# Performance work log

Hardware: AMD Instinct MI355X
Metric: run time of the kernel (lower is better)

## Reference

```python
import jax, jax.numpy as jnp
import numpy as np

H, D, EF, NT, ET = 4, 32, 32, 4, 8
N, E = 100000, 1600000
NEG_SLOPE = 0.2


def setup_inputs() -> dict:
    key = jax.random.key(0)
    ks = jax.random.split(key, 11)
    return {
        "feat": jax.random.normal(ks[0], (N, H * D), jnp.float32),
        "fc": jax.random.normal(ks[1], (NT, H, D), jnp.float32) * 0.1,
        "edge_emb": jax.random.normal(ks[2], (ET, EF), jnp.float32),
        "W_e": jax.random.normal(ks[3], (H * EF, EF), jnp.float32) * 0.1,
        "attn_l": jax.random.normal(ks[4], (1, H, D), jnp.float32) * 0.1,
        "attn_r": jax.random.normal(ks[5], (1, H, D), jnp.float32) * 0.1,
        "attn_e": jax.random.normal(ks[6], (1, H, EF), jnp.float32) * 0.1,
        "node_types": jax.random.randint(ks[7], (N,), 0, NT, jnp.int32),
        "e_feat": jax.random.randint(ks[8], (E,), 0, ET, jnp.int32),
        "src": jax.random.randint(ks[9], (E,), 0, N, jnp.int32),
        "dst": jax.random.randint(ks[10], (E,), 0, N, jnp.int32),
    }


def reference(feat, fc, edge_emb, W_e, attn_l, attn_r, attn_e, node_types, e_feat, src, dst):
    n = feat.shape[0]
    h = feat.reshape(n, H, D)                      # [N,H,D] (h_src == h_dst)
    fs = h * fc[node_types]                        # per-node-type scaling, feat_src == feat_dst

    # edge-type embedding path: Embedding -> Linear(edge_feats, H*edge_feats) -> attn_e score
    emb = (edge_emb @ W_e.T).reshape(ET, H, EF)    # [ET,H,EF]
    ee = (emb * attn_e).sum(-1)[e_feat]            # [E,H]

    el = (fs * attn_l).sum(-1)                     # [N,H]
    er = (fs * attn_r).sum(-1)                     # [N,H]
    e = jax.nn.leaky_relu(el[src] + er[dst] + ee, NEG_SLOPE)  # [E,H]

    # edge_softmax: segment softmax over destination node
    m = jax.ops.segment_max(e, dst, num_segments=n)           # [N,H]
    ex = jnp.exp(e - m[dst])
    s = jax.ops.segment_sum(ex, dst, num_segments=n)          # [N,H]
    a = ex / s[dst]                                            # [E,H]

    # u_mul_e + sum aggregation
    msg = fs[src] * a[:, :, None]                              # [E,H,D]
    rst = jax.ops.segment_sum(msg, dst, num_segments=n)       # [N,H,D]

    rst = rst + h                                              # residual (Identity, in==out feats)
    return rst, a[:, :, None]
```

## Files before the change

kernel.cpp:

```cpp
#include <hip/hip_runtime.h>
#include <stdint.h>

namespace {
constexpr int kH = 4, kD = 32, kEF = 32, kNT = 4, kET = 8;
constexpr int kHD = kH * kD;
constexpr float kNegSlope = 0.2f;
constexpr int kNB = 782;
constexpr int kHB = 512;
constexpr int kXP = 20;

using f32x2 = __attribute__((ext_vector_type(2))) float;

__device__ __forceinline__ float lrelu(float x) { return x > 0.f ? x : kNegSlope * x; }

__global__ void __launch_bounds__(256) k_init(
    const float* __restrict__ feat, const float* __restrict__ fc,
    const float* __restrict__ edge_emb, const float* __restrict__ W_e,
    const float* __restrict__ attn_l, const float* __restrict__ attn_r,
    const float* __restrict__ attn_e, const int* __restrict__ node_types,
    float* __restrict__ el, float* __restrict__ er, uint8_t* __restrict__ fs,
    float* __restrict__ ee_tab, int N) {
  if (blockIdx.x == 0 && threadIdx.x < kET * kH) {
    int et = threadIdx.x / kH, h = threadIdx.x % kH;
    float acc = 0.f;
    for (int f = 0; f < kEF; ++f) {
      const float* wrow = W_e + (h * kEF + f) * kEF;
      const float* erow = edge_emb + et * kEF;
      float emb = 0.f;
      for (int k = 0; k < kEF; ++k) emb += erow[k] * wrow[k];
      acc += emb * attn_e[h * kEF + f];
    }
    ee_tab[et * kH + h] = acc;
  }
  int gid = blockIdx.x * blockDim.x + threadIdx.x;
  int node = gid >> 5;
  int lane = threadIdx.x & 31;
  if (node >= N) return;
  int nt = node_types[node];
  float4 f4 = *(const float4*)(feat + (size_t)(node << 7) + lane * 4);
  float4 c4 = *(const float4*)(fc + nt * kHD + lane * 4);
  float4 al = *(const float4*)(attn_l + lane * 4);
  float4 ar = *(const float4*)(attn_r + lane * 4);
  float fx = f4.x * c4.x, fy = f4.y * c4.y, fz = f4.z * c4.z, fw = f4.w * c4.w;
  int w = __builtin_amdgcn_cvt_pk_fp8_f32(fx, fy, 0, false);
  w = __builtin_amdgcn_cvt_pk_fp8_f32(fz, fw, w, true);
  *(int*)(fs + (size_t)(node << 7) + lane * 4) = w;
  float pl = fx * al.x + fy * al.y + fz * al.z + fw * al.w;
  float pr = fx * ar.x + fy * ar.y + fz * ar.z + fw * ar.w;
#pragma unroll
  for (int off = 1; off < 8; off <<= 1) {
    pl += __shfl_xor(pl, off);
    pr += __shfl_xor(pr, off);
  }
  if ((lane & 7) == 0) {
    int h = lane >> 3;
    el[node * kH + h] = pl;
    er[node * kH + h] = pr;
  }
}

__global__ void __launch_bounds__(256) k_hist(const int* __restrict__ dst,
                                              int* __restrict__ partial, int E) {
  __shared__ int h[kNB];
  for (int i = threadIdx.x; i < kNB; i += 256) h[i] = 0;
  __syncthreads();
  int per = (E + gridDim.x - 1) / gridDim.x;
  int e0 = blockIdx.x * per;
  int e1 = min(e0 + per, E);
  for (int i = e0 + threadIdx.x; i < e1; i += 256) atomicAdd(&h[dst[i] >> 7], 1);
  __syncthreads();
  for (int i = threadIdx.x; i < kNB; i += 256) partial[blockIdx.x * kNB + i] = h[i];
}

__global__ void __launch_bounds__(256) k_scanA(int* __restrict__ partial,
                                               int* __restrict__ btot) {
  __shared__ int bufa[kHB], bufb[kHB];
  int b = blockIdx.x, t = threadIdx.x;
  bufa[t] = partial[t * kNB + b];
  bufa[t + 256] = partial[(t + 256) * kNB + b];
  __syncthreads();
  int* cur = bufa;
  int* nxt = bufb;
  for (int off = 1; off < kHB; off <<= 1) {
    for (int i = t; i < kHB; i += 256) nxt[i] = cur[i] + (i >= off ? cur[i - off] : 0);
    __syncthreads();
    int* sw = cur; cur = nxt; nxt = sw;
  }
  partial[t * kNB + b] = t ? cur[t - 1] : 0;
  partial[(t + 256) * kNB + b] = cur[t + 255];
  if (t == 0) btot[b] = cur[kHB - 1];
}

__global__ void __launch_bounds__(1024) k_scanB(const int* __restrict__ btot,
                                                int* __restrict__ bbase) {
  __shared__ int bufa[1024], bufb[1024];
  int t = threadIdx.x;
  bufa[t] = (t < kNB) ? btot[t] : 0;
  __syncthreads();
  int* cur = bufa;
  int* nxt = bufb;
  for (int off = 1; off < 1024; off <<= 1) {
    nxt[t] = cur[t] + (t >= off ? cur[t - off] : 0);
    __syncthreads();
    int* sw = cur; cur = nxt; nxt = sw;
  }
  if (t < kNB) bbase[t] = t ? cur[t - 1] : 0;
  if (t == kNB - 1) bbase[kNB] = cur[t];
}

__global__ void __launch_bounds__(256) k_scatter2(
    const int* __restrict__ dst, const int* __restrict__ src,
    const int* __restrict__ e_feat, const int* __restrict__ partial,
    const int* __restrict__ bbase, int* __restrict__ tmp, int E) {
  __shared__ int h[kNB];
  for (int i = threadIdx.x; i < kNB; i += 256) h[i] = 0;
  __syncthreads();
  int per = (E + gridDim.x - 1) / gridDim.x;
  int e0 = blockIdx.x * per;
  int e1 = min(e0 + per, E);
  const int* myrow = partial + blockIdx.x * kNB;
  for (int i = e0 + threadIdx.x; i < e1; i += 256) {
    int d = dst[i];
    int b = d >> 7;
    int lr = atomicAdd(&h[b], 1);
    int pos = bbase[b] + myrow[b] + lr;
    tmp[pos] = src[i] | (e_feat[i] << 17) | ((d & 127) << 20);
  }
}

__global__ void __launch_bounds__(256) k_build(const int* __restrict__ bbase,
                                               const int* __restrict__ tmp,
                                               int* __restrict__ ptr,
                                               int* __restrict__ csr, int N, int E) {
  __shared__ int fh[128], fb[128], sc[128];
  int b = blockIdx.x, t = threadIdx.x;
  int s0 = bbase[b], s1 = bbase[b + 1];
  if (t < 128) fh[t] = 0;
  __syncthreads();
  for (int j = s0 + t; j < s1; j += 256) atomicAdd(&fh[tmp[j] >> 20], 1);
  __syncthreads();
  if (t < 128) sc[t] = fh[t];
  __syncthreads();
  for (int off = 1; off < 128; off <<= 1) {
    int v = 0;
    if (t < 128 && t >= off) v = sc[t - off];
    __syncthreads();
    if (t < 128) sc[t] += v;
    __syncthreads();
  }
  if (t < 128) {
    fb[t] = sc[t] - fh[t];
    int d = (b << 7) + t;
    if (d < N) ptr[d] = s0 + fb[t];
    fh[t] = 0;
  }
  if (b == gridDim.x - 1 && t == 0) ptr[N] = E;
  __syncthreads();
  for (int j = s0 + t; j < s1; j += 256) {
    int v = tmp[j];
    int dl = v >> 20;
    int r = atomicAdd(&fh[dl], 1);
    csr[s0 + fb[dl] + r] = v & 0xFFFFF;
  }
}

__global__ void __launch_bounds__(256) k_fused(
    const uint8_t* __restrict__ fs, const float* __restrict__ feat,
    const float* __restrict__ el, const float* __restrict__ er,
    const float* __restrict__ ee_tab, const int* __restrict__ ptr,
    const int* __restrict__ csr, float* __restrict__ rst,
    float* __restrict__ rinv_buf, int N) {
  __shared__ float ee_sh[kET * kH];
  __shared__ __align__(16) float xp[4][64 * kXP];
  if (threadIdx.x < kET * kH) ee_sh[threadIdx.x] = ee_tab[threadIdx.x];
  __syncthreads();
  int lane = threadIdx.x & 63;
  int wid = threadIdx.x >> 6;
  int node = blockIdx.x * 4 + wid;
  bool nvalid = node < N;
  int nodec = nvalid ? node : 0;
  int start = 0, end = 0;
  if (nvalid) {
    start = ptr[node];
    end = ptr[node + 1];
  }

  int g = lane >> 3;
  int q = lane & 7;
  int head = q >> 1;
  int qoff = q << 4;
  float er_h = er[nodec * kH + head];

  float sm = 0.f;
  f32x2 acc[8];
#pragma unroll
  for (int k = 0; k < 8; ++k) acc[k] = (f32x2){0.f, 0.f};

  int j = start + g;
  int pk0 = csr[(j < end) ? j : 0];
  int s0 = pk0 & 0x1FFFF;
  float elv0 = el[(s0 << 2) + head];
  int4 w0 = *(const int4*)(fs + (size_t)(s0 << 7) + qoff);
  float ee0 = ee_sh[((pk0 >> 17) << 2) + head];
  int pk1 = csr[(j + 8 < end) ? j + 8 : 0];

  while (j < end) {
    int s1 = pk1 & 0x1FFFF;
    float elv1 = el[(s1 << 2) + head];
    int4 w1 = *(const int4*)(fs + (size_t)(s1 << 7) + qoff);
    float ee1 = ee_sh[((pk1 >> 17) << 2) + head];
    int pk2 = csr[(j + 16 < end) ? j + 16 : 0];
    float ex = __expf(lrelu(elv0 + er_h + ee0));
    sm += ex;
    f32x2 ex2 = {ex, ex};
#pragma unroll
    for (int c = 0; c < 4; ++c) {
      int wc = c == 0 ? w0.x : c == 1 ? w0.y : c == 2 ? w0.z : w0.w;
      acc[2 * c + 0] += ex2 * __builtin_amdgcn_cvt_pk_f32_fp8(wc, false);
      acc[2 * c + 1] += ex2 * __builtin_amdgcn_cvt_pk_f32_fp8(wc, true);
    }
    elv0 = elv1;
    w0 = w1;
    ee0 = ee1;
    pk1 = pk2;
    j += 8;
  }

  sm += __shfl_xor(sm, 8);
  sm += __shfl_xor(sm, 16);
  sm += __shfl_xor(sm, 32);
  float rinv = sm > 0.f ? 1.f / sm : 0.f;

  float* row = &xp[wid][lane * kXP];
#pragma unroll
  for (int c = 0; c < 4; ++c) {
    float4 v4 = {acc[2 * c].x, acc[2 * c].y, acc[2 * c + 1].x, acc[2 * c + 1].y};
    *(float4*)(row + c * 4) = v4;
  }
  __syncthreads();
  int qsrc = lane >> 3;
  int coff = (lane & 7) * 2;
  const float* base = &xp[wid][qsrc * kXP + coff];
  f32x2 v = {0.f, 0.f};
#pragma unroll
  for (int gg = 0; gg < 8; ++gg) v += *(const f32x2*)(base + gg * 8 * kXP);

  float rs = __shfl(rinv, (lane >> 4) << 1);
  float rb = __shfl(rinv, lane << 1);
  f32x2 f2 = *(const f32x2*)(feat + (size_t)(nodec << 7) + lane * 2);
  f32x2 o = v * rs + f2;
  if (nvalid) {
    *(f32x2*)(rst + (size_t)(node << 7) + lane * 2) = o;
    if (lane < kH) rinv_buf[node * kH + lane] = rb;
  }
}

__global__ void k_post(const int* __restrict__ src, const int* __restrict__ dst,
                       const int* __restrict__ e_feat, const float* __restrict__ el,
                       const float* __restrict__ er, const float* __restrict__ ee_tab,
                       const float* __restrict__ rinv_buf, float* __restrict__ out_a,
                       int E) {
  int i = blockIdx.x * blockDim.x + threadIdx.x;
  if (i >= E) return;
  int s = src[i], d = dst[i], et = e_feat[i];
  float4 elv = *(const float4*)(el + s * kH);
  float4 erv = *(const float4*)(er + d * kH);
  float4 ee = *(const float4*)(ee_tab + et * kH);
  float4 rv = *(const float4*)(rinv_buf + d * kH);
  float4 a;
  a.x = __expf(lrelu(elv.x + erv.x + ee.x)) * rv.x;
  a.y = __expf(lrelu(elv.y + erv.y + ee.y)) * rv.y;
  a.z = __expf(lrelu(elv.z + erv.z + ee.z)) * rv.z;
  a.w = __expf(lrelu(elv.w + erv.w + ee.w)) * rv.w;
  *(float4*)(out_a + (size_t)i * kH) = a;
}

}

extern "C" void kernel_launch(void* const* d_in, const int* in_sizes, int n_in,
                              void* d_out, int out_size, void* d_ws, size_t ws_size,
                              hipStream_t stream) {
  const float* feat = (const float*)d_in[0];
  const float* fc = (const float*)d_in[1];
  const float* edge_emb = (const float*)d_in[2];
  const float* W_e = (const float*)d_in[3];
  const float* attn_l = (const float*)d_in[4];
  const float* attn_r = (const float*)d_in[5];
  const float* attn_e = (const float*)d_in[6];
  const int* node_types = (const int*)d_in[7];
  const int* e_feat = (const int*)d_in[8];
  const int* src = (const int*)d_in[9];
  const int* dst = (const int*)d_in[10];
  int N = in_sizes[7];
  int E = in_sizes[8];

  char* ws = (char*)d_ws;
  size_t off = 0;
  auto alloc = [&](size_t bytes) -> void* {
    void* p = ws + off;
    off = (off + bytes + 255) & ~(size_t)255;
    return p;
  };
  float* ee_tab = (float*)alloc((size_t)kET * kH * sizeof(float));
  float* el = (float*)alloc((size_t)N * kH * sizeof(float));
  float* er = (float*)alloc((size_t)N * kH * sizeof(float));
  float* rinv_buf = (float*)alloc((size_t)N * kH * sizeof(float));
  uint8_t* fs = (uint8_t*)alloc((size_t)N * kHD * sizeof(uint8_t));
  int* partial = (int*)alloc((size_t)kHB * kNB * sizeof(int));
  int* btot = (int*)alloc((size_t)kNB * sizeof(int));
  int* bbase = (int*)alloc((size_t)(kNB + 1) * sizeof(int));
  int* ptr = (int*)alloc((size_t)(N + 1) * sizeof(int));
  int* tmp = (int*)alloc((size_t)E * sizeof(int));
  int* csr = (int*)alloc((size_t)E * sizeof(int));

  k_init<<<(N + 7) / 8, 256, 0, stream>>>(feat, fc, edge_emb, W_e, attn_l, attn_r,
                                          attn_e, node_types, el, er, fs, ee_tab, N);
  k_hist<<<kHB, 256, 0, stream>>>(dst, partial, E);
  k_scanA<<<kNB, 256, 0, stream>>>(partial, btot);
  k_scanB<<<1, 1024, 0, stream>>>(btot, bbase);
  k_scatter2<<<kHB, 256, 0, stream>>>(dst, src, e_feat, partial, bbase, tmp, E);
  k_build<<<kNB, 256, 0, stream>>>(bbase, tmp, ptr, csr, N, E);

  float* rst = (float*)d_out;
  float* out_a = (float*)d_out + (size_t)N * kHD;
  k_fused<<<(N + 3) / 4, 256, 0, stream>>>(fs, feat, el, er, ee_tab, ptr, csr, rst,
                                           rinv_buf, N);
  k_post<<<(E + 255) / 256, 256, 0, stream>>>(src, dst, e_feat, el, er, ee_tab,
                                              rinv_buf, out_a, E);
}
```

Baseline: 307.3 us.

## Drop scanB kernel, deepen gather prefetch, interleave er/rinv, nontemporal stores

Removes the single-block scanB launch by recomputing the block-base prefix inside k_scatter2 (a redundant per-block scan) and inside k_build (a per-block reduction). Deepens the CSR gather prefetch in k_fused from one to two edges ahead. Packs er and rinv into one interleaved per-node buffer so k_post fetches both with adjacent loads. It also swaps the block barrier for an LDS waitcnt, returns early for invalid nodes, and uses nontemporal stores for the outputs. The trade-off is redundant scan work in every block, higher register pressure, and reliance on wave-local LDS ordering being correct without a barrier.

After: 303.2 us. Within noise of the previous version (-1.3%).

```diff
diff --git a/kernel.cpp b/kernel.cpp
--- a/kernel.cpp
+++ b/kernel.cpp
@@ -5,11 +5,13 @@
 constexpr int kH = 4, kD = 32, kEF = 32, kNT = 4, kET = 8;
 constexpr int kHD = kH * kD;
 constexpr float kNegSlope = 0.2f;
-constexpr int kNB = 782;
+constexpr int kBN = 128;
+constexpr int kNB = (100000 + kBN - 1) / kBN;
 constexpr int kHB = 512;
 constexpr int kXP = 20;
 
 using f32x2 = __attribute__((ext_vector_type(2))) float;
+using f32x4 = __attribute__((ext_vector_type(4))) float;
 
 __device__ __forceinline__ float lrelu(float x) { return x > 0.f ? x : kNegSlope * x; }
 
@@ -18,7 +20,7 @@
     const float* __restrict__ edge_emb, const float* __restrict__ W_e,
     const float* __restrict__ attn_l, const float* __restrict__ attn_r,
     const float* __restrict__ attn_e, const int* __restrict__ node_types,
-    float* __restrict__ el, float* __restrict__ er, uint8_t* __restrict__ fs,
+    float* __restrict__ el, float* __restrict__ ernv, uint8_t* __restrict__ fs,
     float* __restrict__ ee_tab, int N) {
   if (blockIdx.x == 0 && threadIdx.x < kET * kH) {
     int et = threadIdx.x / kH, h = threadIdx.x % kH;
@@ -55,7 +57,7 @@
   if ((lane & 7) == 0) {
     int h = lane >> 3;
     el[node * kH + h] = pl;
-    er[node * kH + h] = pr;
+    ernv[(node << 3) + h] = pr;
   }
 }
 
@@ -91,50 +93,56 @@
   if (t == 0) btot[b] = cur[kHB - 1];
 }
 
-__global__ void __launch_bounds__(1024) k_scanB(const int* __restrict__ btot,
-                                                int* __restrict__ bbase) {
-  __shared__ int bufa[1024], bufb[1024];
-  int t = threadIdx.x;
-  bufa[t] = (t < kNB) ? btot[t] : 0;
-  __syncthreads();
-  int* cur = bufa;
-  int* nxt = bufb;
-  for (int off = 1; off < 1024; off <<= 1) {
-    nxt[t] = cur[t] + (t >= off ? cur[t - off] : 0);
-    __syncthreads();
-    int* sw = cur; cur = nxt; nxt = sw;
-  }
-  if (t < kNB) bbase[t] = t ? cur[t - 1] : 0;
-  if (t == kNB - 1) bbase[kNB] = cur[t];
-}
-
 __global__ void __launch_bounds__(256) k_scatter2(
     const int* __restrict__ dst, const int* __restrict__ src,
     const int* __restrict__ e_feat, const int* __restrict__ partial,
-    const int* __restrict__ bbase, int* __restrict__ tmp, int E) {
-  __shared__ int h[kNB];
-  for (int i = threadIdx.x; i < kNB; i += 256) h[i] = 0;
+    const int* __restrict__ btot, int* __restrict__ tmp, int E) {
+  __shared__ int h[kNB], sA[kNB], sB[kNB], bb[kNB];
+  int t = threadIdx.x;
+  for (int i = t; i < kNB; i += 256) sA[i] = btot[i];
+  __syncthreads();
+  int* cur = sA;
+  int* nxt = sB;
+  for (int off = 1; off < kNB; off <<= 1) {
+    for (int i = t; i < kNB; i += 256) nxt[i] = cur[i] + (i >= off ? cur[i - off] : 0);
+    __syncthreads();
+    int* sw = cur; cur = nxt; nxt = sw;
+  }
+  for (int i = t; i < kNB; i += 256) {
+    bb[i] = i ? cur[i - 1] : 0;
+    h[i] = 0;
+  }
   __syncthreads();
   int per = (E + gridDim.x - 1) / gridDim.x;
   int e0 = blockIdx.x * per;
   int e1 = min(e0 + per, E);
   const int* myrow = partial + blockIdx.x * kNB;
-  for (int i = e0 + threadIdx.x; i < e1; i += 256) {
+  for (int i = e0 + t; i < e1; i += 256) {
     int d = dst[i];
     int b = d >> 7;
     int lr = atomicAdd(&h[b], 1);
-    int pos = bbase[b] + myrow[b] + lr;
+    int pos = bb[b] + myrow[b] + lr;
     tmp[pos] = src[i] | (e_feat[i] << 17) | ((d & 127) << 20);
   }
 }
 
-__global__ void __launch_bounds__(256) k_build(const int* __restrict__ bbase,
+__global__ void __launch_bounds__(256) k_build(const int* __restrict__ btot,
                                                const int* __restrict__ tmp,
                                                int* __restrict__ ptr,
                                                int* __restrict__ csr, int N, int E) {
   __shared__ int fh[128], fb[128], sc[128];
+  __shared__ int red[256];
   int b = blockIdx.x, t = threadIdx.x;
-  int s0 = bbase[b], s1 = bbase[b + 1];
+  int acc = 0;
+  for (int i = t; i < b; i += 256) acc += btot[i];
+  red[t] = acc;
+  __syncthreads();
+  for (int off = 128; off > 0; off >>= 1) {
+    if (t < off) red[t] += red[t + off];
+    __syncthreads();
+  }
+  int s0 = red[0];
+  int s1 = s0 + btot[b];
   if (t < 128) fh[t] = 0;
   __syncthreads();
   for (int j = s0 + t; j < s1; j += 256) atomicAdd(&fh[tmp[j] >> 20], 1);
@@ -166,10 +174,9 @@
 
 __global__ void __launch_bounds__(256) k_fused(
     const uint8_t* __restrict__ fs, const float* __restrict__ feat,
-    const float* __restrict__ el, const float* __restrict__ er,
+    const float* __restrict__ el, float* __restrict__ ernv,
     const float* __restrict__ ee_tab, const int* __restrict__ ptr,
-    const int* __restrict__ csr, float* __restrict__ rst,
-    float* __restrict__ rinv_buf, int N) {
+    const int* __restrict__ csr, float* __restrict__ rst, int N) {
   __shared__ float ee_sh[kET * kH];
   __shared__ __align__(16) float xp[4][64 * kXP];
   if (threadIdx.x < kET * kH) ee_sh[threadIdx.x] = ee_tab[threadIdx.x];
@@ -177,19 +184,15 @@
   int lane = threadIdx.x & 63;
   int wid = threadIdx.x >> 6;
   int node = blockIdx.x * 4 + wid;
-  bool nvalid = node < N;
-  int nodec = nvalid ? node : 0;
-  int start = 0, end = 0;
-  if (nvalid) {
-    start = ptr[node];
-    end = ptr[node + 1];
-  }
+  if (node >= N) return;
+  int start = ptr[node], end = ptr[node + 1];
 
   int g = lane >> 3;
   int q = lane & 7;
   int head = q >> 1;
   int qoff = q << 4;
-  float er_h = er[nodec * kH + head];
+  float er_h = ernv[(node << 3) + head];
+  f32x2 f2 = *(const f32x2*)(feat + ((size_t)node << 7) + lane * 2);
 
   float sm = 0.f;
   f32x2 acc[8];
@@ -198,18 +201,23 @@
 
   int j = start + g;
   int pk0 = csr[(j < end) ? j : 0];
+  int pk1 = csr[(j + 8 < end) ? j + 8 : 0];
   int s0 = pk0 & 0x1FFFF;
   float elv0 = el[(s0 << 2) + head];
-  int4 w0 = *(const int4*)(fs + (size_t)(s0 << 7) + qoff);
+  int4 w0 = *(const int4*)(fs + ((size_t)s0 << 7) + qoff);
   float ee0 = ee_sh[((pk0 >> 17) << 2) + head];
-  int pk1 = csr[(j + 8 < end) ? j + 8 : 0];
+  int s1 = pk1 & 0x1FFFF;
+  float elv1 = el[(s1 << 2) + head];
+  int4 w1 = *(const int4*)(fs + ((size_t)s1 << 7) + qoff);
+  float ee1 = ee_sh[((pk1 >> 17) << 2) + head];
+  int pk2 = csr[(j + 16 < end) ? j + 16 : 0];
 
   while (j < end) {
-    int s1 = pk1 & 0x1FFFF;
-    float elv1 = el[(s1 << 2) + head];
-    int4 w1 = *(const int4*)(fs + (size_t)(s1 << 7) + qoff);
-    float ee1 = ee_sh[((pk1 >> 17) << 2) + head];
-    int pk2 = csr[(j + 16 < end) ? j + 16 : 0];
+    int s2 = pk2 & 0x1FFFF;
+    float elv2 = el[(s2 << 2) + head];
+    int4 w2 = *(const int4*)(fs + ((size_t)s2 << 7) + qoff);
+    float ee2 = ee_sh[((pk2 >> 17) << 2) + head];
+    int pk3 = csr[(j + 24 < end) ? j + 24 : 0];
     float ex = __expf(lrelu(elv0 + er_h + ee0));
     sm += ex;
     f32x2 ex2 = {ex, ex};
@@ -219,10 +227,9 @@
       acc[2 * c + 0] += ex2 * __builtin_amdgcn_cvt_pk_f32_fp8(wc, false);
       acc[2 * c + 1] += ex2 * __builtin_amdgcn_cvt_pk_f32_fp8(wc, true);
     }
-    elv0 = elv1;
-    w0 = w1;
-    ee0 = ee1;
-    pk1 = pk2;
+    elv0 = elv1; w0 = w1; ee0 = ee1;
+    elv1 = elv2; w1 = w2; ee1 = ee2;
+    pk2 = pk3;
     j += 8;
   }
 
@@ -237,7 +244,8 @@
     float4 v4 = {acc[2 * c].x, acc[2 * c].y, acc[2 * c + 1].x, acc[2 * c + 1].y};
     *(float4*)(row + c * 4) = v4;
   }
-  __syncthreads();
+  asm volatile("s_waitcnt lgkmcnt(0)" ::: "memory");
+  __builtin_amdgcn_sched_barrier(0);
   int qsrc = lane >> 3;
   int coff = (lane & 7) * 2;
   const float* base = &xp[wid][qsrc * kXP + coff];
@@ -247,32 +255,29 @@
 
   float rs = __shfl(rinv, (lane >> 4) << 1);
   float rb = __shfl(rinv, lane << 1);
-  f32x2 f2 = *(const f32x2*)(feat + (size_t)(nodec << 7) + lane * 2);
   f32x2 o = v * rs + f2;
-  if (nvalid) {
-    *(f32x2*)(rst + (size_t)(node << 7) + lane * 2) = o;
-    if (lane < kH) rinv_buf[node * kH + lane] = rb;
-  }
-}
-
-__global__ void k_post(const int* __restrict__ src, const int* __restrict__ dst,
-                       const int* __restrict__ e_feat, const float* __restrict__ el,
-                       const float* __restrict__ er, const float* __restrict__ ee_tab,
-                       const float* __restrict__ rinv_buf, float* __restrict__ out_a,
-                       int E) {
+  __builtin_nontemporal_store(o, (f32x2*)(rst + ((size_t)node << 7) + lane * 2));
+  if (lane < kH) ernv[(node << 3) + 4 + lane] = rb;
+}
+
+__global__ void __launch_bounds__(256) k_post(
+    const int* __restrict__ src, const int* __restrict__ dst,
+    const int* __restrict__ e_feat, const float* __restrict__ el,
+    const float* __restrict__ ernv, const float* __restrict__ ee_tab,
+    float* __restrict__ out_a, int E) {
   int i = blockIdx.x * blockDim.x + threadIdx.x;
   if (i >= E) return;
   int s = src[i], d = dst[i], et = e_feat[i];
   float4 elv = *(const float4*)(el + s * kH);
-  float4 erv = *(const float4*)(er + d * kH);
+  float4 erv = *(const float4*)(ernv + ((size_t)d << 3));
+  float4 rv = *(const float4*)(ernv + ((size_t)d << 3) + 4);
   float4 ee = *(const float4*)(ee_tab + et * kH);
-  float4 rv = *(const float4*)(rinv_buf + d * kH);
-  float4 a;
+  f32x4 a;
   a.x = __expf(lrelu(elv.x + erv.x + ee.x)) * rv.x;
   a.y = __expf(lrelu(elv.y + erv.y + ee.y)) * rv.y;
   a.z = __expf(lrelu(elv.z + erv.z + ee.z)) * rv.z;
   a.w = __expf(lrelu(elv.w + erv.w + ee.w)) * rv.w;
-  *(float4*)(out_a + (size_t)i * kH) = a;
+  __builtin_nontemporal_store(a, (f32x4*)(out_a + (size_t)i * kH));
 }
 
 }
@@ -303,28 +308,25 @@
   };
   float* ee_tab = (float*)alloc((size_t)kET * kH * sizeof(float));
   float* el = (float*)alloc((size_t)N * kH * sizeof(float));
-  float* er = (float*)alloc((size_t)N * kH * sizeof(float));
-  float* rinv_buf = (float*)alloc((size_t)N * kH * sizeof(float));
+  float* ernv = (float*)alloc((size_t)N * 2 * kH * sizeof(float));
   uint8_t* fs = (uint8_t*)alloc((size_t)N * kHD * sizeof(uint8_t));
   int* partial = (int*)alloc((size_t)kHB * kNB * sizeof(int));
   int* btot = (int*)alloc((size_t)kNB * sizeof(int));
-  int* bbase = (int*)alloc((size_t)(kNB + 1) * sizeof(int));
   int* ptr = (int*)alloc((size_t)(N + 1) * sizeof(int));
   int* tmp = (int*)alloc((size_t)E * sizeof(int));
   int* csr = (int*)alloc((size_t)E * sizeof(int));
 
   k_init<<<(N + 7) / 8, 256, 0, stream>>>(feat, fc, edge_emb, W_e, attn_l, attn_r,
-                                          attn_e, node_types, el, er, fs, ee_tab, N);
+                                          attn_e, node_types, el, ernv, fs, ee_tab, N);
   k_hist<<<kHB, 256, 0, stream>>>(dst, partial, E);
   k_scanA<<<kNB, 256, 0, stream>>>(partial, btot);
-  k_scanB<<<1, 1024, 0, stream>>>(btot, bbase);
-  k_scatter2<<<kHB, 256, 0, stream>>>(dst, src, e_feat, partial, bbase, tmp, E);
-  k_build<<<kNB, 256, 0, stream>>>(bbase, tmp, ptr, csr, N, E);
+  k_scatter2<<<kHB, 256, 0, stream>>>(dst, src, e_feat, partial, btot, tmp, E);
+  k_build<<<kNB, 256, 0, stream>>>(btot, tmp, ptr, csr, N, E);
 
   float* rst = (float*)d_out;
   float* out_a = (float*)d_out + (size_t)N * kHD;
-  k_fused<<<(N + 3) / 4, 256, 0, stream>>>(fs, feat, el, er, ee_tab, ptr, csr, rst,
-                                           rinv_buf, N);
-  k_post<<<(E + 255) / 256, 256, 0, stream>>>(src, dst, e_feat, el, er, ee_tab,
-                                              rinv_buf, out_a, E);
-}
+  k_fused<<<(N + 3) / 4, 256, 0, stream>>>(fs, feat, el, ernv, ee_tab, ptr, csr,
+                                           rst, N);
+  k_post<<<(E + 255) / 256, 256, 0, stream>>>(src, dst, e_feat, el, ernv, ee_tab,
+                                              out_a, E);
+}
```
